# Kernel tuning notes

Hardware: AMD Instinct MI355X
Metric: run time of the kernel (lower is better)

The kernel has to match this reference:

```python
import jax, jax.numpy as jnp
import numpy as np

B, V, F = 32, 1024, 16
A, P, NF = 32, 64, 128
C = P + A  # propagated feature width after concat with edge weights
D_OUT_IN = F + A + 2 * A * C  # 6192, input dim of output Dense


def setup_inputs() -> dict:
    key = jax.random.key(0)
    ks = jax.random.split(key, 4)
    return {
        "x": jax.random.normal(ks[0], (B, V, F), dtype=jnp.float32),
        "W_flr": jax.random.normal(ks[1], (F, P), dtype=jnp.float32) * (1.0 / np.sqrt(F)),
        "b_flr": jnp.zeros((P,), dtype=jnp.float32),
        "W_s": jax.random.normal(ks[2], (F, A), dtype=jnp.float32) * (1.0 / np.sqrt(F)),
        "b_s": jnp.zeros((A,), dtype=jnp.float32),
        "W_out": jax.random.normal(ks[3], (D_OUT_IN, NF), dtype=jnp.float32) * (1.0 / np.sqrt(D_OUT_IN)),
        "b_out": jnp.zeros((NF,), dtype=jnp.float32),
    }


def reference(x, W_flr, b_flr, W_s, b_s, W_out, b_out):
    # Per-vertex transforms
    feat = x @ W_flr + b_flr                      # (B,V,P)
    dist = x @ W_s + b_s                          # (B,V,A)
    ew = jnp.exp(-jnp.square(dist))               # (B,V,A) edge weights vertex->aggregator
    f = jnp.concatenate([feat, ew], axis=-1)      # (B,V,C)

    # Weighted broadcast then vertex-axis reduction (aggregator gather)
    w = jnp.transpose(ew, (0, 2, 1))              # (B,A,V)
    prod = w[..., None] * f[:, None, :, :]        # (B,A,V,C)
    agg_max = jnp.max(prod, axis=2)               # (B,A,C)
    agg_mean = jnp.mean(prod, axis=2)             # (B,A,C)
    agg = jnp.concatenate([agg_max, agg_mean], axis=-1)  # (B,A,2C)

    # Scatter aggregated features back to vertices, weighted by same edge weights
    upd = ew[..., None] * agg[:, None, :, :]      # (B,V,A,2C)
    upd = upd.reshape(B, V, A * 2 * C)            # (B,V,2AC)

    cat = jnp.concatenate([x, upd, ew], axis=-1)  # (B,V,F+2AC+A)
    return jnp.tanh(cat @ W_out + b_out)          # (B,V,NF)
```

## Files before the change

kernel.cpp:

```cpp
#include <hip/hip_runtime.h>
#include <math.h>

#define NB 32
#define NV 1024
#define NFT 16
#define NA 32
#define NP 64
#define NOUT 128
#define NC 96
#define NC2 192

#define NSPLIT 16
#define VPB 64

__global__ void k2p(const float* __restrict__ x,
                    const float* __restrict__ W_flr,
                    const float* __restrict__ b_flr,
                    const float* __restrict__ W_s,
                    const float* __restrict__ b_s,
                    float* __restrict__ ewbuf,
                    float* __restrict__ part) {
    __shared__ float xs[VPB][NFT];
    __shared__ float fs[VPB][NC];

    int b = blockIdx.x, vs = blockIdx.y, tid = threadIdx.x;
    int rowbase = b * NV + vs * VPB;

    {
        const float4* xsrc = (const float4*)(x + (size_t)rowbase * NFT);
        ((float4*)xs)[tid] = xsrc[tid];
    }
    __syncthreads();

    {
        int c  = tid & 127;
        int rh = tid >> 7;
        if (c < NC) {
            float Wcol[NFT], bias;
            if (c < NP) {
                bias = b_flr[c];
#pragma unroll
                for (int k = 0; k < NFT; ++k) Wcol[k] = W_flr[k * NP + c];
            } else {
                int a = c - NP;
                bias = b_s[a];
#pragma unroll
                for (int k = 0; k < NFT; ++k) Wcol[k] = W_s[k * NA + a];
            }
#pragma unroll
            for (int r0 = 0; r0 < 32; ++r0) {
                int r = rh * 32 + r0;
                float xr[NFT];
#pragma unroll
                for (int q = 0; q < 4; ++q)
                    ((float4*)xr)[q] = ((const float4*)xs[r])[q];
                float acc = bias;
#pragma unroll
                for (int k = 0; k < NFT; ++k)
                    acc = fmaf(xr[k], Wcol[k], acc);
                if (c >= NP) {
                    acc = __expf(-acc * acc);
                    ewbuf[(size_t)(rowbase + r) * NA + (c - NP)] = acc;
                }
                fs[r][c] = acc;
            }
        }
    }
    __syncthreads();

    int at = tid >> 5, ct = tid & 31;
    int cbase = ct * 3;
    float sm[4][3], mx[4][3];
#pragma unroll
    for (int i = 0; i < 4; ++i)
#pragma unroll
        for (int j = 0; j < 3; ++j) { sm[i][j] = 0.f; mx[i][j] = -INFINITY; }

    for (int r = 0; r < VPB; ++r) {
        float4 e4 = *(const float4*)&fs[r][NP + at * 4];
        float f0 = fs[r][cbase], f1 = fs[r][cbase + 1], f2 = fs[r][cbase + 2];
        float ee[4] = {e4.x, e4.y, e4.z, e4.w};
#pragma unroll
        for (int i = 0; i < 4; ++i) {
            float p0 = ee[i] * f0, p1 = ee[i] * f1, p2 = ee[i] * f2;
            sm[i][0] += p0; sm[i][1] += p1; sm[i][2] += p2;
            mx[i][0] = fmaxf(mx[i][0], p0);
            mx[i][1] = fmaxf(mx[i][1], p1);
            mx[i][2] = fmaxf(mx[i][2], p2);
        }
    }

    float* pb = part + (size_t)((b * NSPLIT + vs) * NA) * NC2;
#pragma unroll
    for (int i = 0; i < 4; ++i) {
        int a = at * 4 + i;
#pragma unroll
        for (int j = 0; j < 3; ++j) {
            pb[a * NC2 + cbase + j]      = mx[i][j];
            pb[a * NC2 + NC + cbase + j] = sm[i][j];
        }
    }
}

__global__ void k23(const float* __restrict__ part,
                    const float* __restrict__ W_out,
                    float* __restrict__ Gp) {
    __shared__ float aggL[NC2];
    int b = blockIdx.x, a = blockIdx.y, tid = threadIdx.x;

    {
        const float* pb = part + (size_t)(b * NSPLIT * NA + a) * NC2 + tid;
        const size_t stride = (size_t)NA * NC2;
        if (tid < NC) {
            float m = -INFINITY;
#pragma unroll
            for (int vsi = 0; vsi < NSPLIT; ++vsi)
                m = fmaxf(m, pb[vsi * stride]);
            aggL[tid] = m;
        } else {
            float s = 0.f;
#pragma unroll
            for (int vsi = 0; vsi < NSPLIT; ++vsi)
                s += pb[vsi * stride];
            aggL[tid] = s * (1.0f / (float)NV);
        }
    }
    __syncthreads();

    if (tid < NOUT) {
        int n = tid;
        const float* wr = W_out + (size_t)(NFT + a * NC2) * NOUT + n;
        float acc = W_out[(size_t)(NFT + NA * NC2 + a) * NOUT + n];
#pragma unroll 8
        for (int c = 0; c < NC2; ++c)
            acc = fmaf(aggL[c], wr[(size_t)c * NOUT], acc);
        Gp[(size_t)(b * NA + a) * NOUT + n] = acc;
    }
}

#define K4_ROWS 32
__global__ void k4_out(const float* __restrict__ x,
                       const float* __restrict__ ewbuf,
                       const float* __restrict__ Gp,
                       const float* __restrict__ W_out,
                       const float* __restrict__ b_out,
                       float* __restrict__ out) {
    __shared__ float xs[K4_ROWS][NFT];
    __shared__ float es[K4_ROWS][NA];

    int b     = blockIdx.x;
    int chunk = blockIdx.y;
    int tid   = threadIdx.x;
    int n  = tid & (NOUT - 1);
    int rg = tid >> 7;

    int rowbase = b * NV + chunk * K4_ROWS;

    {
        const float4* esrc = (const float4*)(ewbuf + (size_t)rowbase * NA);
        ((float4*)es)[tid] = esrc[tid];
        if (tid < 128) {
            const float4* xsrc = (const float4*)(x + (size_t)rowbase * NFT);
            ((float4*)xs)[tid] = xsrc[tid];
        }
    }

    float Wc[NFT], Gc[NA];
#pragma unroll
    for (int k = 0; k < NFT; ++k)
        Wc[k] = W_out[(size_t)k * NOUT + n];
    const float* gpb = Gp + ((size_t)b * NA) * NOUT + n;
#pragma unroll
    for (int a = 0; a < NA; ++a)
        Gc[a] = gpb[(size_t)a * NOUT];
    float bn = b_out[n];

    __syncthreads();

    float* orow = out + ((size_t)rowbase + rg * 16) * NOUT + n;
#pragma unroll
    for (int r = 0; r < 16; ++r) {
        int row = rg * 16 + r;
        float xr[NFT], er[NA];
#pragma unroll
        for (int q = 0; q < 4; ++q)
            ((float4*)xr)[q] = ((const float4*)xs[row])[q];
#pragma unroll
        for (int q = 0; q < 8; ++q)
            ((float4*)er)[q] = ((const float4*)es[row])[q];

        float s = bn;
#pragma unroll
        for (int k = 0; k < NFT; ++k)
            s = fmaf(xr[k], Wc[k], s);
#pragma unroll
        for (int a = 0; a < NA; ++a)
            s = fmaf(er[a], Gc[a], s);
        s = fminf(fmaxf(s, -15.f), 15.f);
        float e = __expf(2.f * s);
        orow[(size_t)r * NOUT] = (e - 1.f) * __builtin_amdgcn_rcpf(e + 1.f);
    }
}

extern "C" void kernel_launch(void* const* d_in, const int* in_sizes, int n_in,
                              void* d_out, int out_size, void* d_ws, size_t ws_size,
                              hipStream_t stream) {
    const float* x     = (const float*)d_in[0];
    const float* W_flr = (const float*)d_in[1];
    const float* b_flr = (const float*)d_in[2];
    const float* W_s   = (const float*)d_in[3];
    const float* b_s   = (const float*)d_in[4];
    const float* W_out = (const float*)d_in[5];
    const float* b_out = (const float*)d_in[6];
    float* out = (float*)d_out;

    float* ewbuf = (float*)d_ws;
    float* part  = ewbuf + (size_t)NB * NV * NA;
    float* Gp    = part  + (size_t)NB * NSPLIT * NA * NC2;

    {
        dim3 g(NB, NSPLIT);
        k2p<<<g, 256, 0, stream>>>(x, W_flr, b_flr, W_s, b_s, ewbuf, part);
    }
    {
        dim3 g(NB, NA);
        k23<<<g, 192, 0, stream>>>(part, W_out, Gp);
    }
    {
        dim3 g(NB, NV / K4_ROWS);
        k4_out<<<g, 256, 0, stream>>>(x, ewbuf, Gp, W_out, b_out, out);
    }
}
```

Baseline: 42.46 us.

## Compute output projection with bf16 split-precision MFMA instead of scalar FMAs

The final per-vertex projection (x and edge weights against W_out rows and the aggregated Gp matrix) is rewritten as a 64x128xK64 matrix multiply on MFMA units. Inputs are split into high and low bf16 parts and three MFMA products per K-half recover near-fp32 accuracy. Operands are staged in swizzled shared memory to avoid bank conflicts, and K is zero-padded from 48 to 64. The aim is to cut the scalar FMA cost of the output kernel. In exchange it adds conversion work, wasted padded MFMA work, per-block restaging of W_out and Gp, and a small precision risk from dropping the low-by-low term.

Result: faster. 41.19 us (-3.0%).

```diff
diff --git a/kernel.cpp b/kernel.cpp
--- a/kernel.cpp
+++ b/kernel.cpp
@@ -1,4 +1,5 @@
 #include <hip/hip_runtime.h>
+#include <hip/hip_bf16.h>
 #include <math.h>
 
 #define NB 32
@@ -12,6 +13,9 @@
 
 #define NSPLIT 16
 #define VPB 64
+
+typedef __attribute__((ext_vector_type(8))) short bf16x8;
+typedef __attribute__((ext_vector_type(4))) float f32x4;
 
 __global__ void k2p(const float* __restrict__ x,
                     const float* __restrict__ W_flr,
@@ -138,67 +142,151 @@
     }
 }
 
-#define K4_ROWS 32
-__global__ void k4_out(const float* __restrict__ x,
-                       const float* __restrict__ ewbuf,
-                       const float* __restrict__ Gp,
-                       const float* __restrict__ W_out,
-                       const float* __restrict__ b_out,
-                       float* __restrict__ out) {
-    __shared__ float xs[K4_ROWS][NFT];
-    __shared__ float es[K4_ROWS][NA];
-
-    int b     = blockIdx.x;
-    int chunk = blockIdx.y;
-    int tid   = threadIdx.x;
-    int n  = tid & (NOUT - 1);
-    int rg = tid >> 7;
-
-    int rowbase = b * NV + chunk * K4_ROWS;
-
-    {
-        const float4* esrc = (const float4*)(ewbuf + (size_t)rowbase * NA);
-        ((float4*)es)[tid] = esrc[tid];
-        if (tid < 128) {
-            const float4* xsrc = (const float4*)(x + (size_t)rowbase * NFT);
-            ((float4*)xs)[tid] = xsrc[tid];
-        }
-    }
-
-    float Wc[NFT], Gc[NA];
-#pragma unroll
-    for (int k = 0; k < NFT; ++k)
-        Wc[k] = W_out[(size_t)k * NOUT + n];
-    const float* gpb = Gp + ((size_t)b * NA) * NOUT + n;
-#pragma unroll
-    for (int a = 0; a < NA; ++a)
-        Gc[a] = gpb[(size_t)a * NOUT];
-    float bn = b_out[n];
+#define MB 64
+#define SWZ(r, k) (((r) << 6) + ((k) ^ (((r) & 7) << 3)))
+
+__device__ inline void f2hl(float v, ushort& h, ushort& l) {
+    __hip_bfloat16 hb = __float2bfloat16(v);
+    float hf = __bfloat162float(hb);
+    __hip_bfloat16 lb = __float2bfloat16(v - hf);
+    h = *(ushort*)&hb;
+    l = *(ushort*)&lb;
+}
+
+__global__ void k4_mfma(const float* __restrict__ x,
+                        const float* __restrict__ ewbuf,
+                        const float* __restrict__ Gp,
+                        const float* __restrict__ W_out,
+                        const float* __restrict__ b_out,
+                        float* __restrict__ out) {
+    __shared__ ushort AsH[MB * 64], AsL[MB * 64];
+    __shared__ ushort BsH[NOUT * 64], BsL[NOUT * 64];
+    __shared__ float  bs[NOUT];
+
+    int rb = blockIdx.x;
+    int b  = blockIdx.y;
+    int tid = threadIdx.x;
+    int rowbase = b * NV + rb * MB;
+
+    {
+        float4 v = ((const float4*)(x + (size_t)rowbase * NFT))[tid];
+        int r = tid >> 2, kq = (tid & 3) * 4;
+        float vv[4] = {v.x, v.y, v.z, v.w};
+        ushort h[4], l[4];
+#pragma unroll
+        for (int j = 0; j < 4; ++j) f2hl(vv[j], h[j], l[j]);
+        *(uint*)&AsH[SWZ(r, kq)]     = (uint)h[0] | ((uint)h[1] << 16);
+        *(uint*)&AsH[SWZ(r, kq + 2)] = (uint)h[2] | ((uint)h[3] << 16);
+        *(uint*)&AsL[SWZ(r, kq)]     = (uint)l[0] | ((uint)l[1] << 16);
+        *(uint*)&AsL[SWZ(r, kq + 2)] = (uint)l[2] | ((uint)l[3] << 16);
+    }
+    {
+        const float4* es4 = (const float4*)(ewbuf + (size_t)rowbase * NA);
+#pragma unroll
+        for (int t = 0; t < 2; ++t) {
+            int i = tid * 2 + t;
+            float4 v = es4[i];
+            int r = i >> 3, kq = 16 + (i & 7) * 4;
+            float vv[4] = {v.x, v.y, v.z, v.w};
+            ushort h[4], l[4];
+#pragma unroll
+            for (int j = 0; j < 4; ++j) f2hl(vv[j], h[j], l[j]);
+            *(uint*)&AsH[SWZ(r, kq)]     = (uint)h[0] | ((uint)h[1] << 16);
+            *(uint*)&AsH[SWZ(r, kq + 2)] = (uint)h[2] | ((uint)h[3] << 16);
+            *(uint*)&AsL[SWZ(r, kq)]     = (uint)l[0] | ((uint)l[1] << 16);
+            *(uint*)&AsL[SWZ(r, kq + 2)] = (uint)l[2] | ((uint)l[3] << 16);
+        }
+    }
+    {
+#pragma unroll
+        for (int t = 0; t < 2; ++t) {
+            int i = tid * 2 + t;
+            int r = i >> 3, kq = 48 + (i & 7) * 2;
+            *(uint*)&AsH[SWZ(r, kq)] = 0u;
+            *(uint*)&AsL[SWZ(r, kq)] = 0u;
+        }
+    }
+    {
+#pragma unroll
+        for (int t = 0; t < 2; ++t) {
+            int i = tid * 2 + t;
+            int k = i >> 5, nq = (i & 31) * 4;
+            float4 v = ((const float4*)W_out)[i];
+            float vv[4] = {v.x, v.y, v.z, v.w};
+#pragma unroll
+            for (int j = 0; j < 4; ++j) {
+                ushort h, l;
+                f2hl(vv[j], h, l);
+                BsH[SWZ(nq + j, k)] = h;
+                BsL[SWZ(nq + j, k)] = l;
+            }
+        }
+    }
+    {
+        const float4* gp4 = (const float4*)(Gp + (size_t)b * NA * NOUT);
+#pragma unroll
+        for (int t = 0; t < 4; ++t) {
+            int i = tid * 4 + t;
+            int a = i >> 5, nq = (i & 31) * 4;
+            float4 v = gp4[i];
+            int k = 16 + a;
+            float vv[4] = {v.x, v.y, v.z, v.w};
+#pragma unroll
+            for (int j = 0; j < 4; ++j) {
+                ushort h, l;
+                f2hl(vv[j], h, l);
+                BsH[SWZ(nq + j, k)] = h;
+                BsL[SWZ(nq + j, k)] = l;
+            }
+        }
+    }
+    {
+#pragma unroll
+        for (int t = 0; t < 4; ++t) {
+            int i = tid * 4 + t;
+            int n = i >> 3, kq = 48 + (i & 7) * 2;
+            *(uint*)&BsH[SWZ(n, kq)] = 0u;
+            *(uint*)&BsL[SWZ(n, kq)] = 0u;
+        }
+    }
+    if (tid < NOUT) bs[tid] = b_out[tid];
 
     __syncthreads();
 
-    float* orow = out + ((size_t)rowbase + rg * 16) * NOUT + n;
-#pragma unroll
-    for (int r = 0; r < 16; ++r) {
-        int row = rg * 16 + r;
-        float xr[NFT], er[NA];
-#pragma unroll
-        for (int q = 0; q < 4; ++q)
-            ((float4*)xr)[q] = ((const float4*)xs[row])[q];
-#pragma unroll
-        for (int q = 0; q < 8; ++q)
-            ((float4*)er)[q] = ((const float4*)es[row])[q];
-
-        float s = bn;
-#pragma unroll
-        for (int k = 0; k < NFT; ++k)
-            s = fmaf(xr[k], Wc[k], s);
-#pragma unroll
-        for (int a = 0; a < NA; ++a)
-            s = fmaf(er[a], Gc[a], s);
-        s = fminf(fmaxf(s, -15.f), 15.f);
-        float e = __expf(2.f * s);
-        orow[(size_t)r * NOUT] = (e - 1.f) * __builtin_amdgcn_rcpf(e + 1.f);
+    int w = tid >> 6, lane = tid & 63;
+    int r16 = lane & 15, kg = lane >> 4, k0 = kg * 8;
+    int arow = w * 16 + r16;
+
+    bf16x8 AH0 = *(const bf16x8*)&AsH[SWZ(arow, k0)];
+    bf16x8 AH1 = *(const bf16x8*)&AsH[SWZ(arow, 32 + k0)];
+    bf16x8 AL0 = *(const bf16x8*)&AsL[SWZ(arow, k0)];
+    bf16x8 AL1 = *(const bf16x8*)&AsL[SWZ(arow, 32 + k0)];
+
+    int orow0 = rowbase + w * 16 + kg * 4;
+
+#pragma unroll
+    for (int nt = 0; nt < 8; ++nt) {
+        int n = nt * 16 + r16;
+        bf16x8 BH0 = *(const bf16x8*)&BsH[SWZ(n, k0)];
+        bf16x8 BH1 = *(const bf16x8*)&BsH[SWZ(n, 32 + k0)];
+        bf16x8 BL0 = *(const bf16x8*)&BsL[SWZ(n, k0)];
+        bf16x8 BL1 = *(const bf16x8*)&BsL[SWZ(n, 32 + k0)];
+        float bias = bs[n];
+        f32x4 acc = {bias, bias, bias, bias};
+        acc = __builtin_amdgcn_mfma_f32_16x16x32_bf16(AH0, BH0, acc, 0, 0, 0);
+        acc = __builtin_amdgcn_mfma_f32_16x16x32_bf16(AL0, BH0, acc, 0, 0, 0);
+        acc = __builtin_amdgcn_mfma_f32_16x16x32_bf16(AH0, BL0, acc, 0, 0, 0);
+        acc = __builtin_amdgcn_mfma_f32_16x16x32_bf16(AH1, BH1, acc, 0, 0, 0);
+        acc = __builtin_amdgcn_mfma_f32_16x16x32_bf16(AL1, BH1, acc, 0, 0, 0);
+        acc = __builtin_amdgcn_mfma_f32_16x16x32_bf16(AH1, BL1, acc, 0, 0, 0);
+#pragma unroll
+        for (int rg = 0; rg < 4; ++rg) {
+            float s = acc[rg];
+            s = fminf(fmaxf(s, -15.f), 15.f);
+            float e = __expf(2.f * s);
+            out[(size_t)(orow0 + rg) * NOUT + n] =
+                (e - 1.f) * __builtin_amdgcn_rcpf(e + 1.f);
+        }
     }
 }
 
@@ -227,7 +315,7 @@
         k23<<<g, 192, 0, stream>>>(part, W_out, Gp);
     }
     {
-        dim3 g(NB, NV / K4_ROWS);
-        k4_out<<<g, 256, 0, stream>>>(x, ewbuf, Gp, W_out, b_out, out);
-    }
-}
+        dim3 g(NV / MB, NB);
+        k4_mfma<<<g, 256, 0, stream>>>(x, ewbuf, Gp, W_out, b_out, out);
+    }
+}
```
